# Kernel tuning notes

Hardware: AMD Instinct MI355X
Metric: run time of the kernel (lower is better)

Reference implementation:

```python
import jax, jax.numpy as jnp
import numpy as np


def setup_inputs() -> dict:
    key = jax.random.key(0)
    k1, k2 = jax.random.split(key)
    T, H, E = 16384, 4096, 64
    hidden_states = jax.random.normal(k1, (T, H), dtype=jnp.float32)
    W = jax.random.normal(k2, (E, H), dtype=jnp.float32) * 0.02  # init std=0.02
    b = jnp.zeros((E,), dtype=jnp.float32)
    return {"hidden_states": hidden_states, "W": W, "b": b}


def reference(hidden_states, W, b):
    TOPK = 8
    # Linear: [T, H] @ [H, E] + [E] -> [T, E]
    router_logits = jnp.einsum("th,eh->te", hidden_states, W) + b
    router_probs = jax.nn.sigmoid(router_logits)
    routing_weights, routing_indices = jax.lax.top_k(router_probs, TOPK)
    routing_weights = routing_weights / jnp.sum(routing_weights, axis=-1, keepdims=True)
    return routing_weights, routing_indices, router_probs
```

## Files before the change

kernel.cpp:

```cpp
#include <hip/hip_runtime.h>
#include <math.h>

#define H 4096
#define E 64
#define BK 32
#define BM 64
#define TOPK 8

__global__ __launch_bounds__(256) void router_fused_kernel(
    const float* __restrict__ A, const float* __restrict__ Wm,
    const float* __restrict__ bias, float* __restrict__ weights,
    float* __restrict__ indices, float* __restrict__ probs)
{
    __shared__ float  Alds[BM][BK + 4];
    __shared__ float  Wlds[BK][E];
    __shared__ double Llds[BM][E + 1];

    const int tid  = threadIdx.x;
    const int er   = tid & 15;
    const int rr   = tid >> 4;
    const int lrow = tid >> 3;
    const int seg  = tid & 7;

    const long row0 = (long)blockIdx.x * BM;

    double acc[4][4];
#pragma unroll
    for (int i = 0; i < 4; ++i)
#pragma unroll
        for (int j = 0; j < 4; ++j) acc[i][j] = 0.0;

    float4 pa0 = *(const float4*)(A + (row0 + lrow) * H + seg * 4);
    float4 pa1 = *(const float4*)(A + (row0 + lrow + 32) * H + seg * 4);
    float4 pw0 = *(const float4*)(Wm + (long)lrow * H + seg * 4);
    float4 pw1 = *(const float4*)(Wm + (long)(lrow + 32) * H + seg * 4);

    for (int k0 = 0; k0 < H; k0 += BK) {
        *(float4*)&Alds[lrow][seg * 4]      = pa0;
        *(float4*)&Alds[lrow + 32][seg * 4] = pa1;
        Wlds[seg * 4 + 0][lrow] = pw0.x;
        Wlds[seg * 4 + 1][lrow] = pw0.y;
        Wlds[seg * 4 + 2][lrow] = pw0.z;
        Wlds[seg * 4 + 3][lrow] = pw0.w;
        Wlds[seg * 4 + 0][lrow + 32] = pw1.x;
        Wlds[seg * 4 + 1][lrow + 32] = pw1.y;
        Wlds[seg * 4 + 2][lrow + 32] = pw1.z;
        Wlds[seg * 4 + 3][lrow + 32] = pw1.w;
        __syncthreads();

        if (k0 + BK < H) {
            const int kn = k0 + BK;
            pa0 = *(const float4*)(A + (row0 + lrow) * H + kn + seg * 4);
            pa1 = *(const float4*)(A + (row0 + lrow + 32) * H + kn + seg * 4);
            pw0 = *(const float4*)(Wm + (long)lrow * H + kn + seg * 4);
            pw1 = *(const float4*)(Wm + (long)(lrow + 32) * H + kn + seg * 4);
        }

#pragma unroll
        for (int kk = 0; kk < BK; kk += 4) {
            double a[4][4];
            double w[4][4];
#pragma unroll
            for (int i = 0; i < 4; ++i) {
                const float4 t = *(const float4*)&Alds[rr * 4 + i][kk];
                a[i][0] = (double)t.x; a[i][1] = (double)t.y;
                a[i][2] = (double)t.z; a[i][3] = (double)t.w;
            }
#pragma unroll
            for (int m = 0; m < 4; ++m) {
                const float4 t = *(const float4*)&Wlds[kk + m][er * 4];
                w[m][0] = (double)t.x; w[m][1] = (double)t.y;
                w[m][2] = (double)t.z; w[m][3] = (double)t.w;
            }
#pragma unroll
            for (int m = 0; m < 4; ++m)
#pragma unroll
                for (int i = 0; i < 4; ++i)
#pragma unroll
                    for (int j = 0; j < 4; ++j)
                        acc[i][j] = fma(a[i][m], w[m][j], acc[i][j]);
        }
        __syncthreads();
    }

    const float4 bv = *(const float4*)(bias + er * 4);
    const double bb[4] = {(double)bv.x, (double)bv.y, (double)bv.z, (double)bv.w};
#pragma unroll
    for (int i = 0; i < 4; ++i) {
        float4 o;
        float* op = (float*)&o;
#pragma unroll
        for (int j = 0; j < 4; ++j) {
            const double lg = acc[i][j] + bb[j];
            Llds[rr * 4 + i][er * 4 + j] = lg;
            op[j] = 1.0f / (1.0f + __expf(-(float)lg));
        }
        *(float4*)(probs + (row0 + rr * 4 + i) * E + er * 4) = o;
    }
    __syncthreads();

    if (tid < BM) {
        const int r = tid;
        unsigned long long taken = 0ull;
        float wsel[TOPK];
        int   isel[TOPK];
        float sum = 0.0f;
#pragma unroll
        for (int it = 0; it < TOPK; ++it) {
            double best = -1.0e300;
            int    bi   = 0;
            for (int j = 0; j < E; ++j) {
                if (!((taken >> j) & 1ull)) {
                    const double v = Llds[r][j];
                    if (v > best) { best = v; bi = j; }
                }
            }
            taken |= (1ull << bi);
            const float p = 1.0f / (1.0f + __expf(-(float)best));
            wsel[it] = p;
            isel[it] = bi;
            sum += p;
        }
        const float inv = 1.0f / sum;
#pragma unroll
        for (int it = 0; it < TOPK; ++it) {
            weights[(row0 + r) * TOPK + it] = wsel[it] * inv;
            indices[(row0 + r) * TOPK + it] = (float)isel[it];
        }
    }
}

extern "C" void kernel_launch(void* const* d_in, const int* in_sizes, int n_in,
                              void* d_out, int out_size, void* d_ws, size_t ws_size,
                              hipStream_t stream) {
    const float* A    = (const float*)d_in[0];
    const float* W    = (const float*)d_in[1];
    const float* bias = (const float*)d_in[2];
    const int T = in_sizes[0] / H;

    float* out     = (float*)d_out;
    float* weights = out;
    float* indices = out + (size_t)T * TOPK;
    float* probs   = out + (size_t)T * 2 * TOPK;

    hipLaunchKernelGGL(router_fused_kernel, dim3(T / BM), dim3(256), 0, stream,
                       A, W, bias, weights, indices, probs);
}
```

Before: 564.9 us.

## Compute router GEMM in fp32 with wave top-k and fp64 fixup for near-ties

Replaces the fp64 FMA GEMM with an fp32 GEMM using a new tile shape (BM=32, BK=64) and an XOR-swizzled W tile in LDS. Top-k selection moves to wave-wide shuffle reductions, one wave per row. Rows whose top-9 logits have a gap below EPS are recorded through an atomic counter into a list, and a second kernel recomputes those rows in fp64 so the chosen indices still match the reference. This removes the slow fp64 arithmetic, at the cost of two extra kernel launches and a dependence on how often near-ties occur.

```diff
diff --git a/kernel.cpp b/kernel.cpp
--- a/kernel.cpp
+++ b/kernel.cpp
@@ -3,130 +3,172 @@
 
 #define H 4096
 #define E 64
-#define BK 32
-#define BM 64
+#define BK 64
+#define BM 32
 #define TOPK 8
+#define EPS 2e-4f
 
-__global__ __launch_bounds__(256) void router_fused_kernel(
+__global__ void init_cnt_kernel(unsigned int* cnt) {
+    if (threadIdx.x == 0) cnt[0] = 0u;
+}
+
+__global__ __launch_bounds__(256) void router_gemm_kernel(
     const float* __restrict__ A, const float* __restrict__ Wm,
     const float* __restrict__ bias, float* __restrict__ weights,
-    float* __restrict__ indices, float* __restrict__ probs)
+    float* __restrict__ indices, float* __restrict__ probs,
+    unsigned int* __restrict__ cnt, unsigned int* __restrict__ list, int T)
 {
-    __shared__ float  Alds[BM][BK + 4];
-    __shared__ float  Wlds[BK][E];
-    __shared__ double Llds[BM][E + 1];
+    __shared__ float Alds[BM][BK];
+    __shared__ float Wlds[E][BK];
 
     const int tid  = threadIdx.x;
-    const int er   = tid & 15;
-    const int rr   = tid >> 4;
-    const int lrow = tid >> 3;
-    const int seg  = tid & 7;
-
+    const int lane = tid & 63;
+    const int wid  = tid >> 6;
     const long row0 = (long)blockIdx.x * BM;
 
-    double acc[4][4];
+    const int s_row = tid >> 3;
+    const int s_seg = tid & 7;
+    const int w_er  = tid >> 4;
+    const int w_c   = tid & 15;
+
+    float4 acc4[8];
 #pragma unroll
-    for (int i = 0; i < 4; ++i)
+    for (int i = 0; i < 8; ++i) acc4[i] = make_float4(0.f, 0.f, 0.f, 0.f);
+
+    const float* aP = A + (row0 + s_row) * (long)H + s_seg * 4;
+
+    float4 pa0 = *(const float4*)(aP);
+    float4 pa1 = *(const float4*)(aP + 32);
+    float4 pw[4];
 #pragma unroll
-        for (int j = 0; j < 4; ++j) acc[i][j] = 0.0;
-
-    float4 pa0 = *(const float4*)(A + (row0 + lrow) * H + seg * 4);
-    float4 pa1 = *(const float4*)(A + (row0 + lrow + 32) * H + seg * 4);
-    float4 pw0 = *(const float4*)(Wm + (long)lrow * H + seg * 4);
-    float4 pw1 = *(const float4*)(Wm + (long)(lrow + 32) * H + seg * 4);
+    for (int j = 0; j < 4; ++j)
+        pw[j] = *(const float4*)(Wm + (long)(w_er + j * 16) * H + w_c * 4);
 
     for (int k0 = 0; k0 < H; k0 += BK) {
-        *(float4*)&Alds[lrow][seg * 4]      = pa0;
-        *(float4*)&Alds[lrow + 32][seg * 4] = pa1;
-        Wlds[seg * 4 + 0][lrow] = pw0.x;
-        Wlds[seg * 4 + 1][lrow] = pw0.y;
-        Wlds[seg * 4 + 2][lrow] = pw0.z;
-        Wlds[seg * 4 + 3][lrow] = pw0.w;
-        Wlds[seg * 4 + 0][lrow + 32] = pw1.x;
-        Wlds[seg * 4 + 1][lrow + 32] = pw1.y;
-        Wlds[seg * 4 + 2][lrow + 32] = pw1.z;
-        Wlds[seg * 4 + 3][lrow + 32] = pw1.w;
+        *(float4*)&Alds[s_row][s_seg * 4]      = pa0;
+        *(float4*)&Alds[s_row][32 + s_seg * 4] = pa1;
+#pragma unroll
+        for (int j = 0; j < 4; ++j) {
+            const int e  = w_er + j * 16;
+            const int sw = w_c ^ (e & 15);
+            *(float4*)&Wlds[e][sw * 4] = pw[j];
+        }
         __syncthreads();
 
         if (k0 + BK < H) {
             const int kn = k0 + BK;
-            pa0 = *(const float4*)(A + (row0 + lrow) * H + kn + seg * 4);
-            pa1 = *(const float4*)(A + (row0 + lrow + 32) * H + kn + seg * 4);
-            pw0 = *(const float4*)(Wm + (long)lrow * H + kn + seg * 4);
-            pw1 = *(const float4*)(Wm + (long)(lrow + 32) * H + kn + seg * 4);
+            pa0 = *(const float4*)(aP + kn);
+            pa1 = *(const float4*)(aP + kn + 32);
+#pragma unroll
+            for (int j = 0; j < 4; ++j)
+                pw[j] = *(const float4*)(Wm + (long)(w_er + j * 16) * H + kn + w_c * 4);
         }
 
 #pragma unroll
-        for (int kk = 0; kk < BK; kk += 4) {
-            double a[4][4];
-            double w[4][4];
+        for (int g = 0; g < 16; ++g) {
+            const float4 wv = *(const float4*)&Wlds[lane][(g ^ (lane & 15)) * 4];
 #pragma unroll
-            for (int i = 0; i < 4; ++i) {
-                const float4 t = *(const float4*)&Alds[rr * 4 + i][kk];
-                a[i][0] = (double)t.x; a[i][1] = (double)t.y;
-                a[i][2] = (double)t.z; a[i][3] = (double)t.w;
+            for (int i = 0; i < 8; ++i) {
+                const float4 av = *(const float4*)&Alds[wid * 8 + i][g * 4];
+                acc4[i].x = fmaf(av.x, wv.x, acc4[i].x);
+                acc4[i].y = fmaf(av.y, wv.y, acc4[i].y);
+                acc4[i].z = fmaf(av.z, wv.z, acc4[i].z);
+                acc4[i].w = fmaf(av.w, wv.w, acc4[i].w);
             }
-#pragma unroll
-            for (int m = 0; m < 4; ++m) {
-                const float4 t = *(const float4*)&Wlds[kk + m][er * 4];
-                w[m][0] = (double)t.x; w[m][1] = (double)t.y;
-                w[m][2] = (double)t.z; w[m][3] = (double)t.w;
-            }
-#pragma unroll
-            for (int m = 0; m < 4; ++m)
-#pragma unroll
-                for (int i = 0; i < 4; ++i)
-#pragma unroll
-                    for (int j = 0; j < 4; ++j)
-                        acc[i][j] = fma(a[i][m], w[m][j], acc[i][j]);
         }
         __syncthreads();
     }
 
-    const float4 bv = *(const float4*)(bias + er * 4);
-    const double bb[4] = {(double)bv.x, (double)bv.y, (double)bv.z, (double)bv.w};
+    const float bv = bias[lane];
+#pragma unroll 1
+    for (int i = 0; i < 8; ++i) {
+        const long row = row0 + wid * 8 + i;
+        const float logit = (acc4[i].x + acc4[i].y) + (acc4[i].z + acc4[i].w) + bv;
+
+        probs[row * E + lane] = 1.f / (1.f + __expf(-logit));
+
+        float cur = logit;
+        float sv[9]; int si[9];
 #pragma unroll
-    for (int i = 0; i < 4; ++i) {
-        float4 o;
-        float* op = (float*)&o;
+        for (int it = 0; it < 9; ++it) {
+            float bp = cur; int bi = lane;
 #pragma unroll
-        for (int j = 0; j < 4; ++j) {
-            const double lg = acc[i][j] + bb[j];
-            Llds[rr * 4 + i][er * 4 + j] = lg;
-            op[j] = 1.0f / (1.0f + __expf(-(float)lg));
+            for (int off = 32; off >= 1; off >>= 1) {
+                const float op = __shfl_xor(bp, off, 64);
+                const int   oi = __shfl_xor(bi, off, 64);
+                if (op > bp || (op == bp && oi < bi)) { bp = op; bi = oi; }
+            }
+            sv[it] = bp; si[it] = bi;
+            if (lane == bi) cur = -3e38f;
         }
-        *(float4*)(probs + (row0 + rr * 4 + i) * E + er * 4) = o;
-    }
-    __syncthreads();
 
-    if (tid < BM) {
-        const int r = tid;
-        unsigned long long taken = 0ull;
-        float wsel[TOPK];
-        int   isel[TOPK];
-        float sum = 0.0f;
+        float sum = 0.f, mingap = 3e38f;
 #pragma unroll
         for (int it = 0; it < TOPK; ++it) {
-            double best = -1.0e300;
-            int    bi   = 0;
-            for (int j = 0; j < E; ++j) {
-                if (!((taken >> j) & 1ull)) {
-                    const double v = Llds[r][j];
-                    if (v > best) { best = v; bi = j; }
-                }
+            sum += 1.f / (1.f + __expf(-sv[it]));
+            mingap = fminf(mingap, sv[it] - sv[it + 1]);
+        }
+        if (lane < TOPK) {
+            const float p = 1.f / (1.f + __expf(-sv[lane]));
+            weights[row * TOPK + lane] = p / sum;
+            indices[row * TOPK + lane] = (float)si[lane];
+        }
+        if (lane == 0 && mingap < EPS) {
+            const unsigned p = atomicAdd(cnt, 1u);
+            if (p < (unsigned)T) list[p] = (unsigned)row;
+        }
+    }
+}
+
+__global__ __launch_bounds__(256) void fixup_kernel(
+    const float* __restrict__ A, const float* __restrict__ Wm,
+    const float* __restrict__ bias, float* __restrict__ weights,
+    float* __restrict__ indices, const unsigned int* __restrict__ cnt,
+    const unsigned int* __restrict__ list, int T)
+{
+    __shared__ double Llds[E];
+    const int tid = threadIdx.x, lane = tid & 63, wid = tid >> 6;
+    unsigned int count = cnt[0];
+    if (count > (unsigned)T) count = (unsigned)T;
+
+    for (unsigned idx = blockIdx.x; idx < count; idx += gridDim.x) {
+        const long row = (long)list[idx];
+#pragma unroll 1
+        for (int ee = 0; ee < 16; ++ee) {
+            const int e = wid * 16 + ee;
+            double part = 0.0;
+            for (int j = 0; j < 16; ++j) {
+                const int k = j * 256 + lane * 4;
+                const float4 a = *(const float4*)(A + row * H + k);
+                const float4 w = *(const float4*)(Wm + (long)e * H + k);
+                part = fma((double)a.x, (double)w.x, part);
+                part = fma((double)a.y, (double)w.y, part);
+                part = fma((double)a.z, (double)w.z, part);
+                part = fma((double)a.w, (double)w.w, part);
             }
-            taken |= (1ull << bi);
-            const float p = 1.0f / (1.0f + __expf(-(float)best));
-            wsel[it] = p;
-            isel[it] = bi;
-            sum += p;
+#pragma unroll
+            for (int off = 32; off >= 1; off >>= 1)
+                part += __shfl_xor(part, off, 64);
+            if (lane == 0) Llds[e] = part + (double)bias[e];
         }
-        const float inv = 1.0f / sum;
-#pragma unroll
-        for (int it = 0; it < TOPK; ++it) {
-            weights[(row0 + r) * TOPK + it] = wsel[it] * inv;
-            indices[(row0 + r) * TOPK + it] = (float)isel[it];
+        __syncthreads();
+        if (tid == 0) {
+            unsigned long long taken = 0ull;
+            float sv[TOPK]; int si[TOPK]; float sum = 0.f;
+            for (int it = 0; it < TOPK; ++it) {
+                double best = -1.0e300; int bi = 0;
+                for (int j = 0; j < E; ++j)
+                    if (!((taken >> j) & 1ull) && Llds[j] > best) { best = Llds[j]; bi = j; }
+                taken |= 1ull << bi;
+                const float p = 1.f / (1.f + __expf(-(float)best));
+                sv[it] = p; si[it] = bi; sum += p;
+            }
+            for (int it = 0; it < TOPK; ++it) {
+                weights[row * TOPK + it] = sv[it] / sum;
+                indices[row * TOPK + it] = (float)si[it];
+            }
         }
+        __syncthreads();
     }
 }
 
@@ -143,6 +185,12 @@
     float* indices = out + (size_t)T * TOPK;
     float* probs   = out + (size_t)T * 2 * TOPK;
 
-    hipLaunchKernelGGL(router_fused_kernel, dim3(T / BM), dim3(256), 0, stream,
-                       A, W, bias, weights, indices, probs);
+    unsigned int* cnt  = (unsigned int*)d_ws;
+    unsigned int* list = cnt + 8;
+
+    hipLaunchKernelGGL(init_cnt_kernel, dim3(1), dim3(64), 0, stream, cnt);
+    hipLaunchKernelGGL(router_gemm_kernel, dim3(T / BM), dim3(256), 0, stream,
+                       A, W, bias, weights, indices, probs, cnt, list, T);
+    hipLaunchKernelGGL(fixup_kernel, dim3(256), dim3(256), 0, stream,
+                       A, W, bias, weights, indices, cnt, list, T);
 }
```

Result: slower. 795.8 us (+40.9%).
